# Kernel optimization log

Hardware: AMD Instinct MI355X
Metric: run time of the kernel (lower is better)

## Reference

```python
import jax, jax.numpy as jnp
import numpy as np

EPS_AGG = 1e-6  # torch code adds 1e-6 to scatter weight sums
EPS_BN = 1e-5


def _pix_idx(loc_orig, H, W):
    # map normalized coords in [-1,1] to flat pixel index on an HxW grid
    loc = jnp.clip(loc_orig, -1.0, 1.0) * 0.5 + 0.5
    ix = jnp.round(loc[..., 0] * (W - 1)).astype(jnp.int32)
    iy = jnp.round(loc[..., 1] * (H - 1)).astype(jnp.int32)
    return iy * W + ix  # [B, N0]


def token2map(x, loc_orig, idx_agg, H, W):
    # scatter token features to a dense map, averaging collisions
    B, N, C = x.shape
    N0 = idx_agg.shape[1]
    idx_hw = _pix_idx(loc_orig, H, W)                                   # [B, N0]
    tok = jnp.take_along_axis(x, idx_agg[..., None], axis=1)            # [B, N0, C]
    flat = (idx_hw + jnp.arange(B, dtype=jnp.int32)[:, None] * (H * W)).reshape(-1)
    sums = jax.ops.segment_sum(tok.reshape(-1, C), flat, num_segments=B * H * W)
    cnt = jax.ops.segment_sum(jnp.ones((B * N0,), x.dtype), flat, num_segments=B * H * W)
    out = sums / (cnt[:, None] + EPS_AGG)
    return out.reshape(B, H, W, C).transpose(0, 3, 1, 2)                # [B, C, H, W]


def map2token(fmap, Nt, loc_orig, idx_agg_t, agg_weight_t):
    # gather map pixels back to Nt target tokens, weighted-averaging per token
    B, C, H, W = fmap.shape
    idx_hw = _pix_idx(loc_orig, H, W)                                   # [B, N0]
    pix = fmap.transpose(0, 2, 3, 1).reshape(B, H * W, C)
    gath = jnp.take_along_axis(pix, idx_hw[..., None], axis=1)          # [B, N0, C]
    flat = (idx_agg_t + jnp.arange(B, dtype=jnp.int32)[:, None] * Nt).reshape(-1)
    num = jax.ops.segment_sum((gath * agg_weight_t[..., None]).reshape(-1, C), flat, num_segments=B * Nt)
    den = jax.ops.segment_sum(agg_weight_t.reshape(-1), flat, num_segments=B * Nt)
    return (num / (den[:, None] + EPS_AGG)).reshape(B, Nt, C)


def token_downup(x, idx_agg_s, idx_agg_t, agg_weight_t, Nt):
    # weighted aggregation from N source tokens to Nt target tokens via N0 original positions
    B, N, C = x.shape
    src = jnp.take_along_axis(x, idx_agg_s[..., None], axis=1)          # [B, N0, C]
    flat = (idx_agg_t + jnp.arange(B, dtype=jnp.int32)[:, None] * Nt).reshape(-1)
    num = jax.ops.segment_sum((src * agg_weight_t[..., None]).reshape(-1, C), flat, num_segments=B * Nt)
    den = jax.ops.segment_sum(agg_weight_t.reshape(-1), flat, num_segments=B * Nt)
    return (num / (den[:, None] + EPS_AGG)).reshape(B, Nt, C)


def batchnorm(x, gamma, beta):
    # BatchNorm2d on [B,C,Nt,1] == per-channel stats over (B, Nt); x here is [B, Nt, C]
    mu = x.mean(axis=(0, 1), keepdims=True)
    var = x.var(axis=(0, 1), keepdims=True)
    return (x - mu) * jax.lax.rsqrt(var + EPS_BN) * gamma + beta


def setup_inputs() -> dict:
    key = jax.random.key(0)
    ks = jax.random.split(key, 12)
    B, N, N0, Nt, Cin, Cout, H, W = 32, 1568, 3136, 784, 256, 512, 56, 56
    x = jax.random.normal(ks[0], (B, N, Cin), dtype=jnp.float32)
    loc_orig = jax.random.uniform(ks[1], (B, N0, 2), dtype=jnp.float32, minval=-1.0, maxval=1.0)
    idx_agg = jax.random.randint(ks[2], (B, N0), 0, N, dtype=jnp.int32)
    agg_weight = jax.random.uniform(ks[3], (B, N0), dtype=jnp.float32)
    idx_agg_t = jax.random.randint(ks[4], (B, N0), 0, Nt, dtype=jnp.int32)
    agg_weight_t = jax.random.uniform(ks[5], (B, N0), dtype=jnp.float32)
    dw_w = jax.random.normal(ks[6], (Cin, 1, 3, 3), dtype=jnp.float32) * 0.1     # depthwise 3x3
    skip_w = jax.random.normal(ks[7], (Cin,), dtype=jnp.float32) * 0.1           # depthwise 1x1
    conv_w = jax.random.normal(ks[8], (Cout, Cin), dtype=jnp.float32) * (1.0 / np.sqrt(Cin))
    gamma1 = jnp.ones((Cin,), jnp.float32); beta1 = jnp.zeros((Cin,), jnp.float32)
    gamma2 = jnp.ones((Cout,), jnp.float32); beta2 = jnp.zeros((Cout,), jnp.float32)
    return {"x": x, "loc_orig": loc_orig, "idx_agg": idx_agg, "agg_weight": agg_weight,
            "idx_agg_t": idx_agg_t, "agg_weight_t": agg_weight_t, "H": H, "W": W, "Nt": Nt,
            "dw_w": dw_w, "skip_w": skip_w, "conv_w": conv_w,
            "gamma1": gamma1, "beta1": beta1, "gamma2": gamma2, "beta2": beta2}


def reference(x, loc_orig, idx_agg, agg_weight, idx_agg_t, agg_weight_t, H, W, Nt,
              dw_w, skip_w, conv_w, gamma1, beta1, gamma2, beta2):
    # token -> map scatter
    x_map = token2map(x, loc_orig, idx_agg, H, W)                       # [B, Cin, H, W]
    # 3x3 depthwise conv, stride 2, padding 1
    Cin = x_map.shape[1]
    x_map = jax.lax.conv_general_dilated(
        x_map, dw_w, window_strides=(2, 2), padding=((1, 1), (1, 1)),
        feature_group_count=Cin, dimension_numbers=("NCHW", "OIHW", "NCHW"))    # [B, Cin, H/2, W/2]
    # map -> target tokens gather
    x_back = map2token(x_map, Nt, loc_orig, idx_agg_t, agg_weight_t)    # [B, Nt, Cin]
    # skip path: token downsample + 1x1 depthwise (per-channel scale)
    xs = token_downup(x, idx_agg, idx_agg_t, agg_weight_t, Nt)          # [B, Nt, Cin]
    xs = xs * skip_w                                                    # dw_skip, groups=Cin, k=1
    y = xs + x_back
    y = batchnorm(y, gamma1, beta1)
    y = jnp.einsum("bnc,oc->bno", y, conv_w)                            # 1x1 conv Cin->Cout
    y = batchnorm(y, gamma2, beta2)
    return jax.nn.relu(y)                                               # [B, Nt, Cout]
```

## Files before the change

### kernel.cpp

```cpp
#include <hip/hip_runtime.h>

constexpr int B    = 32;
constexpr int N    = 1568;
constexpr int N0   = 3136;
constexpr int Nt   = 784;
constexpr int Cin  = 256;
constexpr int Cout = 512;
constexpr int H    = 56;
constexpr int W    = 56;
constexpr int HW   = 3136;
constexpr int Ho   = 28;
constexpr int Wo   = 28;
constexpr int HWo  = 784;
constexpr int RR   = B * Nt;
constexpr int NE   = B * N0;
constexpr int NBP  = B * HW;
constexpr int NBT  = B * Nt;
constexpr int NB   = NBP + NBT;
constexpr int NCHUNK = NB / 256;

constexpr size_t W_HIST  = 0;
constexpr size_t W_S1SUM = NB;
constexpr size_t W_S1SQ  = W_S1SUM + Cin;
constexpr size_t W_S2SUM = W_S1SQ + Cin;
constexpr size_t W_S2SQ  = W_S2SUM + Cout;
constexpr size_t W_OFF   = NB + 1536;
constexpr size_t W_CUR   = W_OFF + NB + 8;
constexpr size_t W_P56   = W_CUR + NB;
constexpr size_t W_P28   = W_P56 + NE;
constexpr size_t W_BSUM  = W_P28 + NE;
constexpr size_t W_SRTS  = W_BSUM + 512;
constexpr size_t W_STS   = W_SRTS + NE;
constexpr size_t W_STP   = W_STS + NE;
constexpr size_t W_STW   = W_STP + NE;
constexpr size_t W_CONVB = W_STW + NE;
constexpr size_t W_YBF   = W_CONVB + (size_t)B * HWo * Cin / 2;
constexpr size_t W_WFB   = W_YBF + (size_t)RR * Cin / 2;
constexpr size_t W_BIAS  = W_WFB + (size_t)Cout * Cin / 2;
constexpr size_t W_A2    = W_BIAS + Cout;
constexpr size_t W_C2    = W_A2 + Cout;
constexpr size_t W_ZB    = W_C2 + Cout;

__device__ __forceinline__ int pix_of(float t, float scale) {
    t = fminf(fmaxf(t, -1.0f), 1.0f);
    float u = __fadd_rn(__fmul_rn(t, 0.5f), 0.5f);
    return (int)rintf(__fmul_rn(u, scale));
}
__device__ __forceinline__ unsigned short f2bf(float f) {
    unsigned int u = __float_as_uint(f);
    u = (u + 0x7fffu + ((u >> 16) & 1u)) >> 16;
    return (unsigned short)u;
}
__device__ __forceinline__ float bf2f(unsigned short h) {
    return __uint_as_float(((unsigned int)h) << 16);
}

__global__ void k_hist(const float* __restrict__ loc, const int* __restrict__ idxt,
                       int* __restrict__ hist, int* __restrict__ p56a, int* __restrict__ p28a) {
    int i = blockIdx.x * 256 + threadIdx.x;
    if (i >= NE) return;
    int b = i / N0;
    float lx = loc[(size_t)2 * i], ly = loc[(size_t)2 * i + 1];
    int p56 = pix_of(ly, 55.0f) * W + pix_of(lx, 55.0f);
    int p28 = pix_of(ly, 27.0f) * Wo + pix_of(lx, 27.0f);
    p56a[i] = p56; p28a[i] = p28;
    atomicAdd(&hist[b * HW + p56], 1);
    atomicAdd(&hist[NBP + b * Nt + idxt[i]], 1);
}

__global__ void k_scanA(const int* __restrict__ hist, int* __restrict__ bsum) {
    __shared__ int sm[256];
    int i = blockIdx.x * 256 + threadIdx.x;
    sm[threadIdx.x] = hist[i];
    __syncthreads();
    for (int d = 128; d > 0; d >>= 1) {
        if (threadIdx.x < d) sm[threadIdx.x] += sm[threadIdx.x + d];
        __syncthreads();
    }
    if (threadIdx.x == 0) bsum[blockIdx.x] = sm[0];
}

__global__ void k_scanB(int* __restrict__ bsum) {
    __shared__ int sm[512];
    int t = threadIdx.x;
    int v = (t < NCHUNK) ? bsum[t] : 0;
    sm[t] = v; __syncthreads();
    for (int d = 1; d < 512; d <<= 1) {
        int u = (t >= d) ? sm[t - d] : 0;
        __syncthreads();
        sm[t] += u;
        __syncthreads();
    }
    if (t < NCHUNK) bsum[t] = sm[t] - v;
}

__global__ void k_scanC(const int* __restrict__ hist, const int* __restrict__ bsum,
                        int* __restrict__ off, int* __restrict__ cur) {
    __shared__ int sm[256];
    int t = threadIdx.x;
    int i = blockIdx.x * 256 + t;
    int v = hist[i];
    sm[t] = v; __syncthreads();
    for (int d = 1; d < 256; d <<= 1) {
        int u = (t >= d) ? sm[t - d] : 0;
        __syncthreads();
        sm[t] += u;
        __syncthreads();
    }
    int excl = bsum[blockIdx.x] + sm[t] - v;
    off[i] = excl; cur[i] = excl;
    if (i == NB - 1) off[NB] = excl + v;
}

__global__ void k_scatteridx(const int* __restrict__ p56a, const int* __restrict__ p28a,
                             const int* __restrict__ idxa, const int* __restrict__ idxt,
                             const float* __restrict__ wt, int* __restrict__ cur,
                             int* __restrict__ srtS, int* __restrict__ sTs,
                             int* __restrict__ sTp, float* __restrict__ sTw) {
    int i = blockIdx.x * 256 + threadIdx.x;
    if (i >= NE) return;
    int b = i / N0;
    int s = idxa[i];
    int posP = atomicAdd(&cur[b * HW + p56a[i]], 1);
    srtS[posP] = s;
    int posT = atomicAdd(&cur[NBP + b * Nt + idxt[i]], 1) - NE;
    sTs[posT] = s; sTp[posT] = p28a[i]; sTw[posT] = wt[i];
}

constexpr int GCAP = 512;
__global__ __launch_bounds__(256) void k_gconv(const float* __restrict__ x,
        const int* __restrict__ off, const int* __restrict__ srtS,
        const float* __restrict__ dww, unsigned short* __restrict__ convb) {
    __shared__ int   sPk[GCAP];
    __shared__ float sRc[GCAP];
    __shared__ int sSt[9], sCt[9], sPref[10];
    int blk = blockIdx.x;
    int c   = threadIdx.x;
    int b   = blk / HWo;
    int rem = blk - b * HWo;
    int oy  = rem / Wo;
    int ox  = rem - oy * Wo;
    if (c < 9) {
        int ky = c / 3, kx = c - ky * 3;
        int iy = oy * 2 - 1 + ky, ix = ox * 2 - 1 + kx;
        int st = 0, ct = 0;
        if (iy >= 0 && iy < H && ix >= 0 && ix < W) {
            int bin = b * HW + iy * W + ix;
            st = off[bin];
            ct = off[bin + 1] - st;
        }
        sSt[c] = st; sCt[c] = ct;
    }
    __syncthreads();
    if (c == 0) {
        int a = 0;
#pragma unroll
        for (int k = 0; k < 9; ++k) { sPref[k] = a; a += sCt[k]; }
        sPref[9] = a;
    }
    __syncthreads();
    int T = sPref[9];
    float wv[9];
#pragma unroll
    for (int k = 0; k < 9; ++k) wv[k] = dww[c * 9 + k];
    float acc = 0.0f;
    for (int base = 0; base < T; base += GCAP) {
        if (c < 9) {
            int ct = sCt[c], pr = sPref[c], st = sSt[c];
            float rc = 1.0f / ((float)ct + 1e-6f);
            int j0 = max(base - pr, 0);
            int j1 = min(base + GCAP - pr, ct);
            for (int j = j0; j < j1; ++j) {
                sPk[pr + j - base] = srtS[st + j] | (c << 16);
                sRc[pr + j - base] = rc;
            }
        }
        __syncthreads();
        int cnt = min(T - base, GCAP);
        for (int j = 0; j < cnt; ++j) {
            int pk = sPk[j];
            float rc = sRc[j];
            int s = pk & 0xFFFF, tap = pk >> 16;
            acc = fmaf(x[((size_t)b * N + s) * Cin + c] * rc, wv[tap], acc);
        }
        __syncthreads();
    }
    convb[(size_t)blk * Cin + c] = f2bf(acc);
}

constexpr int TCAP = 256;
__global__ __launch_bounds__(256) void k_gtok(const float* __restrict__ x,
        const unsigned short* __restrict__ convb, const int* __restrict__ off,
        const int* __restrict__ sTs, const int* __restrict__ sTp,
        const float* __restrict__ sTw, const float* __restrict__ skipw,
        unsigned short* __restrict__ ybf) {
    __shared__ int sS[TCAP];
    __shared__ int sP[TCAP];
    __shared__ float sW[TCAP];
    int bt = blockIdx.x;
    int c  = threadIdx.x;
    int b  = bt / Nt;
    int st = off[NBP + bt] - NE, en = off[NBP + bt + 1] - NE;
    int T = en - st;
    float sk = skipw[c];
    float acc = 0.0f, wsum = 0.0f;
    for (int base = 0; base < T; base += TCAP) {
        int cnt = min(T - base, TCAP);
        if (c < cnt) {
            sS[c] = sTs[st + base + c];
            sP[c] = sTp[st + base + c];
            sW[c] = sTw[st + base + c];
        }
        __syncthreads();
        for (int j = 0; j < cnt; ++j) {
            int s = sS[j], p = sP[j];
            float w = sW[j];
            wsum += w;
            float cv = bf2f(convb[((size_t)b * HWo + p) * Cin + c]);
            acc = fmaf(w, cv + sk * x[((size_t)b * N + s) * Cin + c], acc);
        }
        __syncthreads();
    }
    ybf[(size_t)bt * Cin + c] = f2bf(acc * (1.0f / (wsum + 1e-6f)));
}

__global__ void k_ystats(const unsigned short* __restrict__ ybf,
                         float* __restrict__ s1, float* __restrict__ s1q) {
    int c = threadIdx.x;
    float sum = 0.0f, sq = 0.0f;
    for (int r = blockIdx.x; r < RR; r += gridDim.x) {
        float v = bf2f(ybf[(size_t)r * Cin + c]);
        sum += v;
        sq = fmaf(v, v, sq);
    }
    atomicAdd(&s1[c], sum);
    atomicAdd(&s1q[c], sq);
}

__global__ void k_fold(const float* __restrict__ s1, const float* __restrict__ s1q,
                       const float* __restrict__ g1, const float* __restrict__ b1,
                       const float* __restrict__ convw, unsigned short* __restrict__ wfb,
                       float* __restrict__ bias) {
    int o = blockIdx.x, c = threadIdx.x;
    const float inv = 1.0f / (float)RR;
    float mu  = s1[c] * inv;
    float var = s1q[c] * inv - mu * mu;
    float a   = g1[c] / sqrtf(var + 1e-5f);
    float bs  = b1[c] - mu * a;
    float wv  = convw[(size_t)o * Cin + c];
    wfb[(size_t)o * Cin + c] = f2bf(wv * a);
    __shared__ float red[256];
    red[c] = wv * bs;
    __syncthreads();
    for (int st = 128; st > 0; st >>= 1) {
        if (c < st) red[c] += red[c + st];
        __syncthreads();
    }
    if (c == 0) bias[o] = red[0];
}

typedef __attribute__((ext_vector_type(8))) short short8;
typedef __attribute__((ext_vector_type(4))) float f32x4;

__global__ __launch_bounds__(256) void k_gemm(const unsigned short* __restrict__ A,
        const unsigned short* __restrict__ Bt, const float* __restrict__ bias,
        unsigned short* __restrict__ zb, float* __restrict__ s2, float* __restrict__ s2q) {
    constexpr int BK = 32, LS = 48;
    __shared__ unsigned short As[128 * LS];
    __shared__ unsigned short Bs[128 * LS];
    __shared__ float rsum[128], rsq[128];
    int m0 = blockIdx.x * 128, n0 = blockIdx.y * 128;
    int t = threadIdx.x;
    int wave = t >> 6, lane = t & 63;
    int wm = wave >> 1, wn = wave & 1;
    int l16 = lane & 15, lq = lane >> 4;
    f32x4 acc[4][4];
#pragma unroll
    for (int i = 0; i < 4; ++i)
#pragma unroll
        for (int j = 0; j < 4; ++j) acc[i][j] = (f32x4)0.0f;
    if (t < 128) { rsum[t] = 0.0f; rsq[t] = 0.0f; }

    for (int k0 = 0; k0 < Cin; k0 += BK) {
#pragma unroll
        for (int r2 = 0; r2 < 2; ++r2) {
            int e = r2 * 256 + t;
            int row = e >> 2, kc = (e & 3) * 8;
            *(float4*)&As[row * LS + kc] = *(const float4*)&A[((size_t)(m0 + row)) * Cin + k0 + kc];
            *(float4*)&Bs[row * LS + kc] = *(const float4*)&Bt[((size_t)(n0 + row)) * Cin + k0 + kc];
        }
        __syncthreads();
        short8 af[4], bf[4];
#pragma unroll
        for (int i = 0; i < 4; ++i) {
            af[i] = *(short8*)&As[(wm * 64 + i * 16 + l16) * LS + lq * 8];
            bf[i] = *(short8*)&Bs[(wn * 64 + i * 16 + l16) * LS + lq * 8];
        }
#pragma unroll
        for (int i = 0; i < 4; ++i)
#pragma unroll
            for (int j = 0; j < 4; ++j)
                acc[i][j] = __builtin_amdgcn_mfma_f32_16x16x32_bf16(af[i], bf[j], acc[i][j], 0, 0, 0);
        __syncthreads();
    }
#pragma unroll
    for (int j = 0; j < 4; ++j) {
        int cl  = wn * 64 + j * 16 + l16;
        int col = n0 + cl;
        float bv = bias[col];
        float ps = 0.0f, pq = 0.0f;
#pragma unroll
        for (int i = 0; i < 4; ++i) {
            int rbase = m0 + wm * 64 + i * 16 + lq * 4;
#pragma unroll
            for (int r = 0; r < 4; ++r) {
                float v = acc[i][j][r] + bv;
                zb[(size_t)(rbase + r) * Cout + col] = f2bf(v);
                ps += v;
                pq = fmaf(v, v, pq);
            }
        }
        atomicAdd(&rsum[cl], ps);
        atomicAdd(&rsq[cl], pq);
    }
    __syncthreads();
    if (t < 128) {
        atomicAdd(&s2[n0 + t], rsum[t]);
        atomicAdd(&s2q[n0 + t], rsq[t]);
    }
}

__global__ void k_fold2(const float* __restrict__ s2, const float* __restrict__ s2q,
                        const float* __restrict__ g2, const float* __restrict__ b2,
                        float* __restrict__ a2, float* __restrict__ c2) {
    int o = threadIdx.x;
    const float inv = 1.0f / (float)RR;
    float mu  = s2[o] * inv;
    float var = s2q[o] * inv - mu * mu;
    float a   = g2[o] / sqrtf(var + 1e-5f);
    a2[o] = a;
    c2[o] = b2[o] - mu * a;
}

__global__ void k_final(const unsigned short* __restrict__ zb, const float* __restrict__ a2,
                        const float* __restrict__ c2, float* __restrict__ out) {
    size_t j4 = ((size_t)blockIdx.x * 256 + threadIdx.x) * 4;
    int o = (int)(j4 & (Cout - 1));
    uint2 u = *(const uint2*)&zb[j4];
    float e0 = bf2f((unsigned short)(u.x & 0xffffu));
    float e1 = bf2f((unsigned short)(u.x >> 16));
    float e2 = bf2f((unsigned short)(u.y & 0xffffu));
    float e3 = bf2f((unsigned short)(u.y >> 16));
    float4 r;
    r.x = fmaxf(fmaf(e0, a2[o + 0], c2[o + 0]), 0.0f);
    r.y = fmaxf(fmaf(e1, a2[o + 1], c2[o + 1]), 0.0f);
    r.z = fmaxf(fmaf(e2, a2[o + 2], c2[o + 2]), 0.0f);
    r.w = fmaxf(fmaf(e3, a2[o + 3], c2[o + 3]), 0.0f);
    *(float4*)&out[j4] = r;
}

extern "C" void kernel_launch(void* const* d_in, const int* in_sizes, int n_in,
                              void* d_out, int out_size, void* d_ws, size_t ws_size,
                              hipStream_t stream) {
    const float* x     = (const float*)d_in[0];
    const float* loc   = (const float*)d_in[1];
    const int*   idxa  = (const int*)d_in[2];
    const int*   idxt  = (const int*)d_in[4];
    const float* wt    = (const float*)d_in[5];
    const float* dww   = (const float*)d_in[9];
    const float* skipw = (const float*)d_in[10];
    const float* convw = (const float*)d_in[11];
    const float* g1    = (const float*)d_in[12];
    const float* b1    = (const float*)d_in[13];
    const float* g2    = (const float*)d_in[14];
    const float* b2    = (const float*)d_in[15];

    float* ws = (float*)d_ws;
    int*   hist  = (int*)(ws + W_HIST);
    float* s1sum = ws + W_S1SUM;
    float* s1sq  = ws + W_S1SQ;
    float* s2sum = ws + W_S2SUM;
    float* s2sq  = ws + W_S2SQ;
    int*   off   = (int*)(ws + W_OFF);
    int*   cur   = (int*)(ws + W_CUR);
    int*   p56a  = (int*)(ws + W_P56);
    int*   p28a  = (int*)(ws + W_P28);
    int*   bsum  = (int*)(ws + W_BSUM);
    int*   srtS  = (int*)(ws + W_SRTS);
    int*   sTs   = (int*)(ws + W_STS);
    int*   sTp   = (int*)(ws + W_STP);
    float* sTw   = ws + W_STW;
    unsigned short* convb = (unsigned short*)(ws + W_CONVB);
    unsigned short* ybf   = (unsigned short*)(ws + W_YBF);
    unsigned short* wfb   = (unsigned short*)(ws + W_WFB);
    float* bias  = ws + W_BIAS;
    float* a2    = ws + W_A2;
    float* c2    = ws + W_C2;
    unsigned short* zb = (unsigned short*)(ws + W_ZB);
    float* out   = (float*)d_out;

    hipMemsetAsync(hist, 0, (size_t)(NB + 1536) * sizeof(float), stream);

    k_hist<<<NE / 256, 256, 0, stream>>>(loc, idxt, hist, p56a, p28a);
    k_scanA<<<NCHUNK, 256, 0, stream>>>(hist, bsum);
    k_scanB<<<1, 512, 0, stream>>>(bsum);
    k_scanC<<<NCHUNK, 256, 0, stream>>>(hist, bsum, off, cur);
    k_scatteridx<<<NE / 256, 256, 0, stream>>>(p56a, p28a, idxa, idxt, wt, cur, srtS, sTs, sTp, sTw);

    k_gconv<<<B * HWo, 256, 0, stream>>>(x, off, srtS, dww, convb);
    k_gtok<<<NBT, 256, 0, stream>>>(x, convb, off, sTs, sTp, sTw, skipw, ybf);
    k_ystats<<<256, 256, 0, stream>>>(ybf, s1sum, s1sq);
    k_fold<<<Cout, 256, 0, stream>>>(s1sum, s1sq, g1, b1, convw, wfb, bias);

    dim3 gg(RR / 128, Cout / 128);
    k_gemm<<<gg, 256, 0, stream>>>(ybf, wfb, bias, zb, s2sum, s2sq);
    k_fold2<<<1, 512, 0, stream>>>(s2sum, s2sq, g2, b2, a2, c2);
    k_final<<<(int)(((size_t)RR * Cout) / 1024), 256, 0, stream>>>(zb, a2, c2, out);
}
```

Measured before the change: 303.1 us.

## Split gather-conv into bf16 scatter-average plus dense depthwise conv, fuse fold2 into final

```diff
diff --git a/kernel.cpp b/kernel.cpp
--- a/kernel.cpp
+++ b/kernel.cpp
@@ -18,6 +18,7 @@
 constexpr int NBT  = B * Nt;
 constexpr int NB   = NBP + NBT;
 constexpr int NCHUNK = NB / 256;
+constexpr size_t XTOT = (size_t)B * N * Cin;
 
 constexpr size_t W_HIST  = 0;
 constexpr size_t W_S1SUM = NB;
@@ -37,9 +38,9 @@
 constexpr size_t W_YBF   = W_CONVB + (size_t)B * HWo * Cin / 2;
 constexpr size_t W_WFB   = W_YBF + (size_t)RR * Cin / 2;
 constexpr size_t W_BIAS  = W_WFB + (size_t)Cout * Cin / 2;
-constexpr size_t W_A2    = W_BIAS + Cout;
-constexpr size_t W_C2    = W_A2 + Cout;
-constexpr size_t W_ZB    = W_C2 + Cout;
+constexpr size_t W_ZB    = W_BIAS + Cout;
+constexpr size_t W_AVG   = W_ZB;
+constexpr size_t W_XH    = W_AVG + (size_t)B * HW * Cin / 2;
 
 __device__ __forceinline__ int pix_of(float t, float scale) {
     t = fminf(fmaxf(t, -1.0f), 1.0f);
@@ -53,6 +54,15 @@
 }
 __device__ __forceinline__ float bf2f(unsigned short h) {
     return __uint_as_float(((unsigned int)h) << 16);
+}
+
+__global__ void k_cast(const float* __restrict__ x, uint2* __restrict__ xh2) {
+    size_t i = (size_t)blockIdx.x * 256 + threadIdx.x;
+    float4 v = *(const float4*)&x[i * 4];
+    uint2 o;
+    o.x = (unsigned int)f2bf(v.x) | ((unsigned int)f2bf(v.y) << 16);
+    o.y = (unsigned int)f2bf(v.z) | ((unsigned int)f2bf(v.w) << 16);
+    xh2[i] = o;
 }
 
 __global__ void k_hist(const float* __restrict__ loc, const int* __restrict__ idxt,
@@ -127,101 +137,106 @@
     sTs[posT] = s; sTp[posT] = p28a[i]; sTw[posT] = wt[i];
 }
 
-constexpr int GCAP = 512;
-__global__ __launch_bounds__(256) void k_gconv(const float* __restrict__ x,
+__global__ __launch_bounds__(256) void k_avg(const unsigned short* __restrict__ xh,
         const int* __restrict__ off, const int* __restrict__ srtS,
+        unsigned int* __restrict__ avg2) {
+    int blk = blockIdx.x;
+    int t = threadIdx.x;
+    int q = t >> 7;
+    int l = t & 127;
+    int bin0 = blk * 4;
+    int b = bin0 / HW;
+    const unsigned int* xb = (const unsigned int*)(xh + (size_t)b * N * Cin) + l;
+#pragma unroll
+    for (int e = 0; e < 2; ++e) {
+        int bin = bin0 + q * 2 + e;
+        int st = off[bin], en = off[bin + 1];
+        float sx = 0.0f, sy = 0.0f;
+        for (int j = st; j < en; ++j) {
+            unsigned int v = xb[(size_t)srtS[j] * 128];
+            sx += bf2f((unsigned short)(v & 0xffffu));
+            sy += bf2f((unsigned short)(v >> 16));
+        }
+        float rc = 1.0f / ((float)(en - st) + 1e-6f);
+        avg2[(size_t)bin * 128 + l] =
+            (unsigned int)f2bf(sx * rc) | ((unsigned int)f2bf(sy * rc) << 16);
+    }
+}
+
+__global__ __launch_bounds__(256) void k_dconv(const unsigned short* __restrict__ avg,
         const float* __restrict__ dww, unsigned short* __restrict__ convb) {
-    __shared__ int   sPk[GCAP];
-    __shared__ float sRc[GCAP];
-    __shared__ int sSt[9], sCt[9], sPref[10];
     int blk = blockIdx.x;
-    int c   = threadIdx.x;
-    int b   = blk / HWo;
-    int rem = blk - b * HWo;
-    int oy  = rem / Wo;
-    int ox  = rem - oy * Wo;
-    if (c < 9) {
-        int ky = c / 3, kx = c - ky * 3;
-        int iy = oy * 2 - 1 + ky, ix = ox * 2 - 1 + kx;
-        int st = 0, ct = 0;
-        if (iy >= 0 && iy < H && ix >= 0 && ix < W) {
-            int bin = b * HW + iy * W + ix;
-            st = off[bin];
-            ct = off[bin + 1] - st;
-        }
-        sSt[c] = st; sCt[c] = ct;
-    }
-    __syncthreads();
-    if (c == 0) {
-        int a = 0;
-#pragma unroll
-        for (int k = 0; k < 9; ++k) { sPref[k] = a; a += sCt[k]; }
-        sPref[9] = a;
-    }
-    __syncthreads();
-    int T = sPref[9];
-    float wv[9];
-#pragma unroll
-    for (int k = 0; k < 9; ++k) wv[k] = dww[c * 9 + k];
-    float acc = 0.0f;
-    for (int base = 0; base < T; base += GCAP) {
-        if (c < 9) {
-            int ct = sCt[c], pr = sPref[c], st = sSt[c];
-            float rc = 1.0f / ((float)ct + 1e-6f);
-            int j0 = max(base - pr, 0);
-            int j1 = min(base + GCAP - pr, ct);
-            for (int j = j0; j < j1; ++j) {
-                sPk[pr + j - base] = srtS[st + j] | (c << 16);
-                sRc[pr + j - base] = rc;
-            }
-        }
-        __syncthreads();
-        int cnt = min(T - base, GCAP);
-        for (int j = 0; j < cnt; ++j) {
-            int pk = sPk[j];
-            float rc = sRc[j];
-            int s = pk & 0xFFFF, tap = pk >> 16;
-            acc = fmaf(x[((size_t)b * N + s) * Cin + c] * rc, wv[tap], acc);
-        }
-        __syncthreads();
-    }
-    convb[(size_t)blk * Cin + c] = f2bf(acc);
-}
-
-constexpr int TCAP = 256;
-__global__ __launch_bounds__(256) void k_gtok(const float* __restrict__ x,
+    int b = blk / Ho, oy = blk - b * Ho;
+    int c = threadIdx.x;
+    float wm[9];
+    const unsigned short* rowb[3];
+#pragma unroll
+    for (int ky = 0; ky < 3; ++ky) {
+        int iy = 2 * oy - 1 + ky;
+        bool ok = (iy >= 0) && (iy < H);
+        int iyc = ok ? iy : 0;
+        rowb[ky] = avg + ((size_t)b * HW + (size_t)iyc * W) * Cin;
+        float m = ok ? 1.0f : 0.0f;
+#pragma unroll
+        for (int kx = 0; kx < 3; ++kx) wm[ky * 3 + kx] = dww[c * 9 + ky * 3 + kx] * m;
+    }
+    size_t obase = ((size_t)b * HWo + (size_t)oy * Wo) * Cin + c;
+    {
+        float acc = 0.0f;
+#pragma unroll
+        for (int ky = 0; ky < 3; ++ky)
+#pragma unroll
+            for (int kx = 1; kx < 3; ++kx)
+                acc = fmaf(bf2f(rowb[ky][(size_t)(kx - 1) * Cin + c]), wm[ky * 3 + kx], acc);
+        convb[obase] = f2bf(acc);
+    }
+#pragma unroll 4
+    for (int ox = 1; ox < 28; ++ox) {
+        float acc = 0.0f;
+#pragma unroll
+        for (int ky = 0; ky < 3; ++ky)
+#pragma unroll
+            for (int kx = 0; kx < 3; ++kx)
+                acc = fmaf(bf2f(rowb[ky][(size_t)(2 * ox - 1 + kx) * Cin + c]),
+                           wm[ky * 3 + kx], acc);
+        convb[obase + (size_t)ox * Cin] = f2bf(acc);
+    }
+}
+
+__global__ __launch_bounds__(256) void k_gtok(const unsigned short* __restrict__ xh,
         const unsigned short* __restrict__ convb, const int* __restrict__ off,
         const int* __restrict__ sTs, const int* __restrict__ sTp,
         const float* __restrict__ sTw, const float* __restrict__ skipw,
-        unsigned short* __restrict__ ybf) {
-    __shared__ int sS[TCAP];
-    __shared__ int sP[TCAP];
-    __shared__ float sW[TCAP];
-    int bt = blockIdx.x;
-    int c  = threadIdx.x;
-    int b  = bt / Nt;
-    int st = off[NBP + bt] - NE, en = off[NBP + bt + 1] - NE;
-    int T = en - st;
-    float sk = skipw[c];
-    float acc = 0.0f, wsum = 0.0f;
-    for (int base = 0; base < T; base += TCAP) {
-        int cnt = min(T - base, TCAP);
-        if (c < cnt) {
-            sS[c] = sTs[st + base + c];
-            sP[c] = sTp[st + base + c];
-            sW[c] = sTw[st + base + c];
+        unsigned int* __restrict__ ybf2) {
+    int blk = blockIdx.x;
+    int t = threadIdx.x;
+    int q = t >> 7;
+    int l = t & 127;
+    int bt0 = blk * 4;
+    int b = bt0 / Nt;
+    const unsigned int* xb = (const unsigned int*)(xh + (size_t)b * N * Cin) + l;
+    const unsigned int* cb = (const unsigned int*)(convb + (size_t)b * HWo * Cin) + l;
+    float2 sk = ((const float2*)skipw)[l];
+#pragma unroll
+    for (int e = 0; e < 2; ++e) {
+        int bt = bt0 + q * 2 + e;
+        int st = off[NBP + bt] - NE, en = off[NBP + bt + 1] - NE;
+        float ax = 0.0f, ay = 0.0f, wsum = 0.0f;
+        for (int j = st; j < en; ++j) {
+            int s = sTs[j], p = sTp[j];
+            float w = sTw[j];
+            unsigned int cv = cb[(size_t)p * 128];
+            unsigned int xv = xb[(size_t)s * 128];
+            wsum += w;
+            ax = fmaf(w, fmaf(sk.x, bf2f((unsigned short)(xv & 0xffffu)),
+                              bf2f((unsigned short)(cv & 0xffffu))), ax);
+            ay = fmaf(w, fmaf(sk.y, bf2f((unsigned short)(xv >> 16)),
+                              bf2f((unsigned short)(cv >> 16))), ay);
         }
-        __syncthreads();
-        for (int j = 0; j < cnt; ++j) {
-            int s = sS[j], p = sP[j];
-            float w = sW[j];
-            wsum += w;
-            float cv = bf2f(convb[((size_t)b * HWo + p) * Cin + c]);
-            acc = fmaf(w, cv + sk * x[((size_t)b * N + s) * Cin + c], acc);
-        }
-        __syncthreads();
-    }
-    ybf[(size_t)bt * Cin + c] = f2bf(acc * (1.0f / (wsum + 1e-6f)));
+        float rw = 1.0f / (wsum + 1e-6f);
+        ybf2[(size_t)bt * 128 + l] =
+            (unsigned int)f2bf(ax * rw) | ((unsigned int)f2bf(ay * rw) << 16);
+    }
 }
 
 __global__ void k_ystats(const unsigned short* __restrict__ ybf,
@@ -330,32 +345,25 @@
     }
 }
 
-__global__ void k_fold2(const float* __restrict__ s2, const float* __restrict__ s2q,
-                        const float* __restrict__ g2, const float* __restrict__ b2,
-                        float* __restrict__ a2, float* __restrict__ c2) {
-    int o = threadIdx.x;
-    const float inv = 1.0f / (float)RR;
-    float mu  = s2[o] * inv;
-    float var = s2q[o] * inv - mu * mu;
-    float a   = g2[o] / sqrtf(var + 1e-5f);
-    a2[o] = a;
-    c2[o] = b2[o] - mu * a;
-}
-
-__global__ void k_final(const unsigned short* __restrict__ zb, const float* __restrict__ a2,
-                        const float* __restrict__ c2, float* __restrict__ out) {
+__global__ void k_final(const unsigned short* __restrict__ zb, const float* __restrict__ s2,
+                        const float* __restrict__ s2q, const float* __restrict__ g2,
+                        const float* __restrict__ b2, float* __restrict__ out) {
     size_t j4 = ((size_t)blockIdx.x * 256 + threadIdx.x) * 4;
     int o = (int)(j4 & (Cout - 1));
+    const float inv = 1.0f / (float)RR;
     uint2 u = *(const uint2*)&zb[j4];
-    float e0 = bf2f((unsigned short)(u.x & 0xffffu));
-    float e1 = bf2f((unsigned short)(u.x >> 16));
-    float e2 = bf2f((unsigned short)(u.y & 0xffffu));
-    float e3 = bf2f((unsigned short)(u.y >> 16));
     float4 r;
-    r.x = fmaxf(fmaf(e0, a2[o + 0], c2[o + 0]), 0.0f);
-    r.y = fmaxf(fmaf(e1, a2[o + 1], c2[o + 1]), 0.0f);
-    r.z = fmaxf(fmaf(e2, a2[o + 2], c2[o + 2]), 0.0f);
-    r.w = fmaxf(fmaf(e3, a2[o + 3], c2[o + 3]), 0.0f);
+#pragma unroll
+    for (int k = 0; k < 4; ++k) {
+        float mu  = s2[o + k] * inv;
+        float var = s2q[o + k] * inv - mu * mu;
+        float a   = g2[o + k] / sqrtf(var + 1e-5f);
+        float cc  = b2[o + k] - mu * a;
+        unsigned short hv = (k < 2) ? (unsigned short)((k & 1) ? (u.x >> 16) : (u.x & 0xffffu))
+                                    : (unsigned short)((k & 1) ? (u.y >> 16) : (u.y & 0xffffu));
+        float v = fmaf(bf2f(hv), a, cc);
+        ((float*)&r)[k] = fmaxf(v, 0.0f);
+    }
     *(float4*)&out[j4] = r;
 }
 
@@ -394,26 +402,27 @@
     unsigned short* ybf   = (unsigned short*)(ws + W_YBF);
     unsigned short* wfb   = (unsigned short*)(ws + W_WFB);
     float* bias  = ws + W_BIAS;
-    float* a2    = ws + W_A2;
-    float* c2    = ws + W_C2;
-    unsigned short* zb = (unsigned short*)(ws + W_ZB);
+    unsigned short* zb  = (unsigned short*)(ws + W_ZB);
+    unsigned short* avg = (unsigned short*)(ws + W_AVG);
+    unsigned short* xh  = (unsigned short*)(ws + W_XH);
     float* out   = (float*)d_out;
 
     hipMemsetAsync(hist, 0, (size_t)(NB + 1536) * sizeof(float), stream);
 
+    k_cast<<<(int)(XTOT / 4 / 256), 256, 0, stream>>>(x, (uint2*)xh);
     k_hist<<<NE / 256, 256, 0, stream>>>(loc, idxt, hist, p56a, p28a);
     k_scanA<<<NCHUNK, 256, 0, stream>>>(hist, bsum);
     k_scanB<<<1, 512, 0, stream>>>(bsum);
     k_scanC<<<NCHUNK, 256, 0, stream>>>(hist, bsum, off, cur);
     k_scatteridx<<<NE / 256, 256, 0, stream>>>(p56a, p28a, idxa, idxt, wt, cur, srtS, sTs, sTp, sTw);
 
-    k_gconv<<<B * HWo, 256, 0, stream>>>(x, off, srtS, dww, convb);
-    k_gtok<<<NBT, 256, 0, stream>>>(x, convb, off, sTs, sTp, sTw, skipw, ybf);
+    k_avg<<<NBP / 4, 256, 0, stream>>>(xh, off, srtS, (unsigned int*)avg);
+    k_dconv<<<B * Ho, 256, 0, stream>>>(avg, dww, convb);
+    k_gtok<<<NBT / 4, 256, 0, stream>>>(xh, convb, off, sTs, sTp, sTw, skipw, (unsigned int*)ybf);
     k_ystats<<<256, 256, 0, stream>>>(ybf, s1sum, s1sq);
     k_fold<<<Cout, 256, 0, stream>>>(s1sum, s1sq, g1, b1, convw, wfb, bias);
 
     dim3 gg(RR / 128, Cout / 128);
     k_gemm<<<gg, 256, 0, stream>>>(ybf, wfb, bias, zb, s2sum, s2sq);
-    k_fold2<<<1, 512, 0, stream>>>(s2sum, s2sq, g2, b2, a2, c2);
-    k_final<<<(int)(((size_t)RR * Cout) / 1024), 256, 0, stream>>>(zb, a2, c2, out);
-}
+    k_final<<<(int)(((size_t)RR * Cout) / 1024), 256, 0, stream>>>(zb, s2sum, s2sq, g2, b2, out);
+}
```

After: 314.2 us. +3.7%, slower.
